# Kernel tuning notes

Hardware: AMD Instinct MI355X
Metric: run time of the kernel (lower is better)

Reference implementation:

```python
import jax, jax.numpy as jnp
import numpy as np

SCALE = 1.0 / np.sqrt(512.0).astype(np.float32)  # attention() hardcodes d_k=512


def setup_inputs() -> dict:
    key = jax.random.key(0)
    ks = jax.random.split(key, 9)
    B, S, D = 4, 2048, 512
    mk = lambda k, shape: jax.random.normal(k, shape, dtype=jnp.float32) * 0.05
    return {
        "q": mk(ks[0], (B, S, D)),
        "k": mk(ks[1], (B, S, D)),
        "v": mk(ks[2], (B, S, D)),
        "WQ_w": mk(ks[3], (D, D)),
        "WQ_b": mk(ks[4], (D,)),
        "WK_w": mk(ks[5], (D, D)),
        "WK_b": mk(ks[6], (D,)),
        "WV_w": mk(ks[7], (D, D)),
        "WV_b": mk(ks[8], (D,)),
    }


def reference(q, k, v, WQ_w, WQ_b, WK_w, WK_b, WV_w, WV_b):
    # torch nn.Linear: y = x @ W.T + b
    qp = q @ WQ_w.T + WQ_b  # [B,S,dk]
    kp = k @ WK_w.T + WK_b  # [B,S,dk]
    vp = v @ WV_w.T + WV_b  # [B,S,dv]
    qk = jnp.einsum("bqd,bkd->bqk", qp, kp) * SCALE  # [B,Sq,Sk]
    S = qk.shape[1]
    tril = jnp.tril(jnp.ones((S, S), dtype=qk.dtype))  # multiplicative causal mask
    qk = qk * tril
    # NOTE: original applies softmax over dim=1 (the query axis), faithfully kept.
    attn = jax.nn.softmax(qk, axis=1)
    out = jnp.einsum("bqk,bkd->bqd", attn, vp)  # [B,Sq,dv]
    return out
```

## Files before the change

### kernel.cpp

```cpp
#include <hip/hip_runtime.h>
#include <hip/hip_bf16.h>


#define S_LEN 2048
#define D_DIM 512
#define SCALE_F 0.044194173824159216f

typedef __attribute__((ext_vector_type(8))) short s8v;
typedef __attribute__((ext_vector_type(4))) short s4v;
typedef __attribute__((ext_vector_type(4))) float f4v;

enum { EPI_BIAS = 0, EPI_BIAS_T = 1, EPI_SCORES = 2 };

#define SBAR()    __builtin_amdgcn_s_barrier()
#define SCHEDB()  __builtin_amdgcn_sched_barrier(0)
#define WAITV(n)  asm volatile("s_waitcnt vmcnt(" #n ")")
#define WAITL0()  asm volatile("s_waitcnt lgkmcnt(0)")

__device__ __forceinline__ short f2bf_s(float f) {
  union { __hip_bfloat16 b; short s; } u; u.b = __float2bfloat16(f); return u.s;
}
__device__ __forceinline__ float bf2f_s(short h) {
  union { short s; __hip_bfloat16 b; } u; u.s = h; return __bfloat162float(u.b);
}

__device__ __forceinline__ void glds16(const short* g, short* l) {
  __builtin_amdgcn_global_load_lds((const __attribute__((address_space(1))) void*)g,
                                   (__attribute__((address_space(3))) void*)l, 16, 0, 0);
}

__device__ __forceinline__ unsigned lds_addr(const short* p) {
  return (unsigned)(unsigned long long)(const __attribute__((address_space(3))) short*)p;
}

__device__ __forceinline__ s8v dsr128(unsigned a) {
  s8v r;
  asm volatile("ds_read_b128 %0, %1" : "=&v"(r) : "v"(a));
  return r;
}

template <int EPI>
__device__ __forceinline__ void gemm_core(
    const short* __restrict__ A, const short* __restrict__ B,
    short* __restrict__ C, const float* __restrict__ bias,
    short* SMEM, int N, int K, size_t sCz, int m0, int n0, int bz,
    float* __restrict__ Z)
{
  const int tid  = threadIdx.x;
  const int w    = tid >> 6;
  const int lane = tid & 63;
  const int quad = lane >> 4;
  const int l16  = lane & 15;
  const int wm   = (w >> 1) * 64;
  const int wn   = (w & 1) * 64;

  const int strow = tid >> 3;
  const int gl = ((tid & 7) ^ (strow & 7)) * 8;

  f4v acc[4][4];
#pragma unroll
  for (int i = 0; i < 4; ++i)
#pragma unroll
    for (int j = 0; j < 4; ++j)
#pragma unroll
      for (int r = 0; r < 4; ++r) acc[i][j][r] = 0.0f;

  const short* Ag = A + (size_t)(m0 + strow) * K + gl;
  const short* Bg = B + (size_t)(n0 + strow) * K + gl;
  const size_t pstr = (size_t)32 * K;
  const int t8 = tid * 8;
  const int swq = l16 & 7;

  const unsigned base = lds_addr(SMEM);
  unsigned aoff[4], boff[4];
#pragma unroll
  for (int ii = 0; ii < 4; ++ii)
    aoff[ii] = base + (unsigned)((wm + ii * 16 + l16) * 128 + ((quad ^ swq) * 16));
#pragma unroll
  for (int j = 0; j < 4; ++j)
    boff[j] = base + 16384u + (unsigned)((wn + j * 16 + l16) * 128 + ((quad ^ swq) * 16));

  const int niter = K >> 6;

#pragma unroll
  for (int p = 0; p < 4; ++p) glds16(Ag + p * pstr, SMEM + t8 + p * 2048);
#pragma unroll
  for (int p = 0; p < 4; ++p) glds16(Bg + p * pstr, SMEM + 8192 + t8 + p * 2048);

  for (int i = 0; i < niter; ++i) {
    const int c = i & 1;
    if (i + 1 < niter) {
      const int k1 = (i + 1) << 6;
      short* dA = SMEM + (1 - c) * 16384 + t8;
#pragma unroll
      for (int p = 0; p < 4; ++p) glds16(Ag + k1 + p * pstr, dA + p * 2048);
#pragma unroll
      for (int p = 0; p < 4; ++p) glds16(Bg + k1 + p * pstr, dA + 8192 + p * 2048);
      SCHEDB();
      WAITV(8);
    } else {
      WAITV(0);
    }
    SBAR();
    SCHEDB();

    const unsigned cofs = (unsigned)(c << 15);
#pragma unroll
    for (int kk = 0; kk < 2; ++kk) {
      const unsigned kx = (unsigned)(kk << 6);
      s8v af[4], bf[4];
#pragma unroll
      for (int ii = 0; ii < 4; ++ii) af[ii] = dsr128((aoff[ii] ^ kx) + cofs);
#pragma unroll
      for (int j = 0; j < 4; ++j)   bf[j]  = dsr128((boff[j] ^ kx) + cofs);
      WAITL0();
      SCHEDB();
      __builtin_amdgcn_s_setprio(1);
#pragma unroll
      for (int ii = 0; ii < 4; ++ii)
#pragma unroll
        for (int j = 0; j < 4; ++j)
          acc[ii][j] = __builtin_amdgcn_mfma_f32_16x16x32_bf16(af[ii], bf[j], acc[ii][j], 0, 0, 0);
      __builtin_amdgcn_s_setprio(0);
    }
    SBAR();
  }

  float bv[4];
  if (EPI == EPI_BIAS || EPI == EPI_BIAS_T) {
#pragma unroll
    for (int j = 0; j < 4; ++j) bv[j] = bias[n0 + wn + j * 16 + l16];
  }

  if (EPI == EPI_BIAS_T) {
#pragma unroll
    for (int i = 0; i < 4; ++i) {
#pragma unroll
      for (int j = 0; j < 4; ++j) {
        const int gn  = n0 + wn + j * 16 + l16;
        const int gmb = m0 + wm + i * 16 + quad * 4;
        const int bb = gmb >> 11, ssb = gmb & (S_LEN - 1);
        s4v o;
#pragma unroll
        for (int r = 0; r < 4; ++r) o[r] = f2bf_s(acc[i][j][r] + bv[j]);
        *(s4v*)&C[((size_t)bb * D_DIM + gn) * S_LEN + ssb] = o;
      }
    }
    return;
  }

  short* TB = SMEM;
  const int wbase = w * 2176;
  float csum[4] = {0.f, 0.f, 0.f, 0.f};

#pragma unroll
  for (int ph = 0; ph < 2; ++ph) {
    __syncthreads();
#pragma unroll
    for (int ii = 0; ii < 2; ++ii) {
      const int i = ph * 2 + ii;
#pragma unroll
      for (int j = 0; j < 4; ++j) {
        const int gn = n0 + wn + j * 16 + l16;
#pragma unroll
        for (int r = 0; r < 4; ++r) {
          short o;
          if (EPI == EPI_SCORES) {
            const int gm = m0 + wm + i * 16 + quad * 4 + r;
            const float f = (gm >= gn) ? (__expf(acc[i][j][r] * SCALE_F) - 1.0f) : 0.0f;
            csum[j] += f;
            o = f2bf_s(f);
          } else {
            o = f2bf_s(acc[i][j][r] + bv[j]);
          }
          TB[wbase + (ii * 16 + quad * 4 + r) * 68 + j * 16 + l16] = o;
        }
      }
    }
    __syncthreads();
#pragma unroll
    for (int p = 0; p < 4; ++p) {
      const int row = p * 8 + (lane >> 3);
      const int cg  = lane & 7;
      const s8v vv = *(const s8v*)&TB[wbase + row * 68 + cg * 8];
      const int gm = m0 + wm + ph * 32 + row;
      const int gn = n0 + wn + cg * 8;
      *(s8v*)&C[sCz + (size_t)gm * N + gn] = vv;
    }
  }

  if (EPI == EPI_SCORES) {
#pragma unroll
    for (int j = 0; j < 4; ++j) {
      float cs = csum[j];
      cs += __shfl_xor(cs, 16, 64);
      cs += __shfl_xor(cs, 32, 64);
      if (quad == 0) atomicAdd(&Z[(bz << 11) + n0 + wn + j * 16 + l16], cs);
    }
  }
}

__global__ __launch_bounds__(256, 2) void proj_qk(
    const short* __restrict__ a0, const short* __restrict__ a1,
    const short* __restrict__ b0, const short* __restrict__ b1,
    short* __restrict__ c0, short* __restrict__ c1,
    const float* __restrict__ x0, const float* __restrict__ x1)
{
  __shared__ __align__(16) short SMEM[32768];
  const int bid = blockIdx.x;
  const int bsw = (bid & 7) * 64 + (bid >> 3);
  const int z   = bsw >> 8;
  const int rem = bsw & 255;
  const int m0  = (rem >> 2) * 128;
  const int n0  = (rem & 3) * 128;
  const short* A = z ? a1 : a0;
  const short* B = z ? b1 : b0;
  short*       C = z ? c1 : c0;
  const float* bias = z ? x1 : x0;
  gemm_core<EPI_BIAS>(A, B, C, bias, SMEM, D_DIM, D_DIM, 0, m0, n0, 0, nullptr);
}

__global__ __launch_bounds__(256, 2) void scores_projv(
    const short* __restrict__ qp, const short* __restrict__ kp, short* __restrict__ F,
    float* __restrict__ Z,
    const short* __restrict__ vb, const short* __restrict__ Wvb,
    short* __restrict__ vpT, const float* __restrict__ xv)
{
  __shared__ __align__(16) short SMEM[32768];
  const int bid = blockIdx.x;
  if (bid < 544) {
    const int bsw = (bid & 7) * 68 + (bid >> 3);
    const int bz  = bsw / 136;
    const int t   = bsw - bz * 136;
    int ti = (int)((sqrtf(8.0f * t + 1.0f) - 1.0f) * 0.5f);
    while ((ti + 1) * (ti + 2) / 2 <= t) ++ti;
    while (ti * (ti + 1) / 2 > t) --ti;
    const int tj = t - ti * (ti + 1) / 2;
    gemm_core<EPI_SCORES>(qp + (size_t)bz * S_LEN * D_DIM, kp + (size_t)bz * S_LEN * D_DIM,
                          F, nullptr, SMEM, S_LEN, D_DIM,
                          (size_t)bz * S_LEN * S_LEN, ti * 128, tj * 128, bz, Z);
  } else {
    const int h   = bid - 544;
    const int hsw = (h & 7) * 32 + (h >> 3);
    const int m0  = (hsw >> 2) * 128;
    const int n0  = (hsw & 3) * 128;
    gemm_core<EPI_BIAS_T>(vb, Wvb, vpT, xv, SMEM, D_DIM, D_DIM, 0, m0, n0, 0, nullptr);
  }
}

__global__ __launch_bounds__(256, 2) void gemm_outF(
    const short* __restrict__ F, const short* __restrict__ vpT,
    const float* __restrict__ Tv, float* __restrict__ out)
{
  __shared__ __align__(16) short SMEM[36864];

  const int tid  = threadIdx.x;
  const int h    = blockIdx.x;
  const int x    = h & 7;
  const int s    = h >> 3;
  const int n0   = (s & 3) * 128;
  const int bz   = (s >> 2) & 3;
  const int zslot = s >> 4;
  const int zs   = (zslot < 2) ? (2 * x + zslot) : (16 + 2 * x + (zslot - 2));
  const int mi   = (zs < 16) ? (31 - zs) : (zs - 16);
  const int m0   = mi * 64;

  const short* A = F   + (size_t)bz * S_LEN * S_LEN;
  const short* B = vpT + (size_t)bz * D_DIM * S_LEN;

  const int w    = tid >> 6;
  const int lane = tid & 63;
  const int quad = lane >> 4;
  const int l16  = lane & 15;
  const int wm   = (w >> 1) * 32;
  const int wn   = (w & 1) * 64;

  const int strow = tid >> 3;
  const int gl = ((tid & 7) ^ (strow & 7)) * 8;

  f4v acc[2][4];
#pragma unroll
  for (int i = 0; i < 2; ++i)
#pragma unroll
    for (int j = 0; j < 4; ++j)
#pragma unroll
      for (int r = 0; r < 4; ++r) acc[i][j][r] = 0.0f;

  const short* Ag = A + (size_t)(m0 + strow) * S_LEN + gl;
  const short* Bg = B + (size_t)(n0 + strow) * S_LEN + gl;
  const size_t pstr = (size_t)32 * S_LEN;
  const int t8 = tid * 8;
  const int swq = l16 & 7;

  const unsigned base = lds_addr(SMEM);
  unsigned aoff[2], boff[4];
#pragma unroll
  for (int ii = 0; ii < 2; ++ii)
    aoff[ii] = base + (unsigned)((wm + ii * 16 + l16) * 128 + ((quad ^ swq) * 16));
#pragma unroll
  for (int j = 0; j < 4; ++j)
    boff[j] = base + 8192u + (unsigned)((wn + j * 16 + l16) * 128 + ((quad ^ swq) * 16));

  const int niter = mi + 1;

#pragma unroll
  for (int pre = 0; pre < 2; ++pre) {
    short* dst = SMEM + pre * 12288 + t8;
    const int k0 = pre << 6;
#pragma unroll
    for (int p = 0; p < 2; ++p) glds16(Ag + k0 + p * pstr, dst + p * 2048);
#pragma unroll
    for (int p = 0; p < 4; ++p) glds16(Bg + k0 + p * pstr, dst + 4096 + p * 2048);
  }

  int cbuf = 0;
  for (int i = 0; i < niter; ++i) {
    if (i + 1 < niter) { WAITV(6); } else { WAITV(0); }
    SBAR();
    SCHEDB();

    if (i + 2 < niter) {
      int nb = cbuf + 2; if (nb >= 3) nb -= 3;
      const int k2 = (i + 2) << 6;
      short* dst = SMEM + nb * 12288 + t8;
#pragma unroll
      for (int p = 0; p < 2; ++p) glds16(Ag + k2 + p * pstr, dst + p * 2048);
#pragma unroll
      for (int p = 0; p < 4; ++p) glds16(Bg + k2 + p * pstr, dst + 4096 + p * 2048);
      SCHEDB();
    }

    const unsigned cofs = (unsigned)(cbuf * 24576);
    cbuf = (cbuf == 2) ? 0 : cbuf + 1;
#pragma unroll
    for (int kk = 0; kk < 2; ++kk) {
      const unsigned kx = (unsigned)(kk << 6);
      s8v af[2], bf[4];
#pragma unroll
      for (int ii = 0; ii < 2; ++ii) af[ii] = dsr128((aoff[ii] ^ kx) + cofs);
#pragma unroll
      for (int j = 0; j < 4; ++j)   bf[j]  = dsr128((boff[j] ^ kx) + cofs);
      WAITL0();
      SCHEDB();
      __builtin_amdgcn_s_setprio(1);
#pragma unroll
      for (int ii = 0; ii < 2; ++ii)
#pragma unroll
        for (int j = 0; j < 4; ++j)
          acc[ii][j] = __builtin_amdgcn_mfma_f32_16x16x32_bf16(af[ii], bf[j], acc[ii][j], 0, 0, 0);
      __builtin_amdgcn_s_setprio(0);
    }
  }

  float* Cf = out + (size_t)bz * S_LEN * D_DIM;
#pragma unroll
  for (int i = 0; i < 2; ++i) {
#pragma unroll
    for (int j = 0; j < 4; ++j) {
      const int gn = n0 + wn + j * 16 + l16;
      const float tvn = Tv[(bz << 9) + gn];
#pragma unroll
      for (int r = 0; r < 4; ++r) {
        const int gm = m0 + wm + i * 16 + quad * 4 + r;
        Cf[(size_t)gm * D_DIM + gn] = acc[i][j][r] + tvn;
      }
    }
  }
}

__global__ __launch_bounds__(256) void cvt_all(
    const float* __restrict__ q, const float* __restrict__ k, const float* __restrict__ v,
    const float* __restrict__ wq, const float* __restrict__ wk, const float* __restrict__ wv,
    short* __restrict__ qb, short* __restrict__ kb, short* __restrict__ vb,
    short* __restrict__ Wqb, short* __restrict__ Wkb, short* __restrict__ Wvb,
    float* __restrict__ ZF)
{
  const int y = blockIdx.y;
  const float* s; short* d; int i;
  if (blockIdx.x < 2048) {
    s = (y == 0) ? q : (y == 1) ? k : v;
    d = (y == 0) ? qb : (y == 1) ? kb : vb;
    i = (blockIdx.x * 256 + threadIdx.x) * 8;
    if (y == 0) {
      const int gid = blockIdx.x * 256 + threadIdx.x;
      if (gid < 8192) ZF[gid] = 0.0f;
    }
  } else {
    s = (y == 0) ? wq : (y == 1) ? wk : wv;
    d = (y == 0) ? Wqb : (y == 1) ? Wkb : Wvb;
    i = ((int)(blockIdx.x - 2048) * 256 + threadIdx.x) * 8;
  }
  const float4 f0 = *(const float4*)(s + i);
  const float4 f1 = *(const float4*)(s + i + 4);
  s8v o;
  o[0] = f2bf_s(f0.x); o[1] = f2bf_s(f0.y); o[2] = f2bf_s(f0.z); o[3] = f2bf_s(f0.w);
  o[4] = f2bf_s(f1.x); o[5] = f2bf_s(f1.y); o[6] = f2bf_s(f1.z); o[7] = f2bf_s(f1.w);
  *(s8v*)(d + i) = o;
}

__global__ __launch_bounds__(256) void scale_vpt_T(
    short* __restrict__ vpT, const float* __restrict__ ZF, float* __restrict__ Tv)
{
  __shared__ float red[4];
  const int b = blockIdx.y, d = blockIdx.x, tid = threadIdx.x;
  const size_t rowbase = ((size_t)(b * D_DIM + d)) * S_LEN;
  const float* zf = ZF + (b << 11);
  const int k0 = tid * 8;

  s8v v = *(s8v*)&vpT[rowbase + k0];
  float s = 0.0f;
#pragma unroll
  for (int i = 0; i < 8; ++i) {
    const float w = bf2f_s(v[i]) / (2048.0f + zf[k0 + i]);
    s += w;
    v[i] = f2bf_s(w);
  }
  *(s8v*)&vpT[rowbase + k0] = v;

#pragma unroll
  for (int off = 32; off >= 1; off >>= 1) s += __shfl_xor(s, off, 64);
  if ((tid & 63) == 0) red[tid >> 6] = s;
  __syncthreads();
  if (tid == 0) Tv[(b << 9) + d] = red[0] + red[1] + red[2] + red[3];
}

extern "C" void kernel_launch(void* const* d_in, const int* in_sizes, int n_in,
                              void* d_out, int out_size, void* d_ws, size_t ws_size,
                              hipStream_t stream) {
  const float* q   = (const float*)d_in[0];
  const float* k   = (const float*)d_in[1];
  const float* v   = (const float*)d_in[2];
  const float* WQw = (const float*)d_in[3];
  const float* WQb = (const float*)d_in[4];
  const float* WKw = (const float*)d_in[5];
  const float* WKb = (const float*)d_in[6];
  const float* WVw = (const float*)d_in[7];
  const float* WVb = (const float*)d_in[8];

  char* ws = (char*)d_ws;
  short* F   = (short*)(ws);
  short* qb  = (short*)(ws);
  short* kb  = qb + 4194304;
  short* Wqb = (short*)(ws + 25165824);
  short* Wkb = Wqb + 262144;
  short* qp  = (short*)(ws + 33554432);
  short* kp  = (short*)(ws + 41943040);
  short* vpT = (short*)(ws + 50331648);
  float* ZF  = (float*)(ws + 58720256);
  float* Tv  = (float*)(ws + 58753024);
  short* vb  = (short*)d_out;
  short* Wvb = (short*)d_out + 4194304;

  const dim3 blk(256);

  cvt_all<<<dim3(2176, 3), blk, 0, stream>>>(
      q, k, v, WQw, WKw, WVw, qb, kb, vb, Wqb, Wkb, Wvb, ZF);

  proj_qk<<<dim3(512), blk, 0, stream>>>(qb, kb, Wqb, Wkb, qp, kp, WQb, WKb);

  scores_projv<<<dim3(800), blk, 0, stream>>>(qp, kp, F, ZF, vb, Wvb, vpT, WVb);

  scale_vpt_T<<<dim3(512, 4), blk, 0, stream>>>(vpT, ZF, Tv);

  gemm_outF<<<dim3(512), blk, 0, stream>>>(F, vpT, Tv, (float*)d_out);
}
```

Baseline: 162.4 us.

## Fuse V-projection scaling and column-sum into scores kernel via completion counter

Removes the separate scale_vpt_T kernel. V-projection blocks in scores_projv now spin-wait on a global counter until all 544 score tiles have finished writing their Z column sums. They then divide by (2048+Z), write bf16 vpT, and atomically accumulate Tv. This saves one launch and a full read/write pass over vpT, but V blocks hold CUs while they wait, and the cross-block spin could stall or hit the guard if blocks are not co-resident.

```diff
diff --git a/kernel.cpp b/kernel.cpp
--- a/kernel.cpp
+++ b/kernel.cpp
@@ -10,7 +10,7 @@
 typedef __attribute__((ext_vector_type(4))) short s4v;
 typedef __attribute__((ext_vector_type(4))) float f4v;
 
-enum { EPI_BIAS = 0, EPI_BIAS_T = 1, EPI_SCORES = 2 };
+enum { EPI_BIAS = 0, EPI_BIAS_T = 1, EPI_SCORES = 2, EPI_BIAS_T_SCALED = 3 };
 
 #define SBAR()    __builtin_amdgcn_s_barrier()
 #define SCHEDB()  __builtin_amdgcn_sched_barrier(0)
@@ -44,7 +44,7 @@
     const short* __restrict__ A, const short* __restrict__ B,
     short* __restrict__ C, const float* __restrict__ bias,
     short* SMEM, int N, int K, size_t sCz, int m0, int n0, int bz,
-    float* __restrict__ Z)
+    float* __restrict__ Z, float* __restrict__ TvP, int* __restrict__ done)
 {
   const int tid  = threadIdx.x;
   const int w    = tid >> 6;
@@ -127,7 +127,7 @@
   }
 
   float bv[4];
-  if (EPI == EPI_BIAS || EPI == EPI_BIAS_T) {
+  if (EPI == EPI_BIAS || EPI == EPI_BIAS_T || EPI == EPI_BIAS_T_SCALED) {
 #pragma unroll
     for (int j = 0; j < 4; ++j) bv[j] = bias[n0 + wn + j * 16 + l16];
   }
@@ -145,6 +145,47 @@
         for (int r = 0; r < 4; ++r) o[r] = f2bf_s(acc[i][j][r] + bv[j]);
         *(s4v*)&C[((size_t)bb * D_DIM + gn) * S_LEN + ssb] = o;
       }
+    }
+    return;
+  }
+
+  if (EPI == EPI_BIAS_T_SCALED) {
+    if (tid == 0) {
+      int guard = 0;
+      while (__hip_atomic_load(done, __ATOMIC_RELAXED, __HIP_MEMORY_SCOPE_AGENT) < 544) {
+        __builtin_amdgcn_s_sleep(8);
+        if (++guard > (1 << 22)) break;
+      }
+      __threadfence();
+    }
+    __syncthreads();
+
+    const int bb  = m0 >> 11;
+    const int kb0 = m0 & (S_LEN - 1);
+    const float* zf = Z + (bb << 11);
+    float csum[4] = {0.f, 0.f, 0.f, 0.f};
+#pragma unroll
+    for (int i = 0; i < 4; ++i) {
+#pragma unroll
+      for (int j = 0; j < 4; ++j) {
+        const int gn  = n0 + wn + j * 16 + l16;
+        const int kk0 = kb0 + wm + i * 16 + quad * 4;
+        s4v o;
+#pragma unroll
+        for (int r = 0; r < 4; ++r) {
+          const float sc = (acc[i][j][r] + bv[j]) / (2048.0f + zf[kk0 + r]);
+          csum[j] += sc;
+          o[r] = f2bf_s(sc);
+        }
+        *(s4v*)&C[((size_t)bb * D_DIM + gn) * S_LEN + kk0] = o;
+      }
+    }
+#pragma unroll
+    for (int j = 0; j < 4; ++j) {
+      float cs = csum[j];
+      cs += __shfl_xor(cs, 16, 64);
+      cs += __shfl_xor(cs, 32, 64);
+      if (quad == 0) atomicAdd(&TvP[(bb << 9) + n0 + wn + j * 16 + l16], cs);
     }
     return;
   }
@@ -217,14 +258,16 @@
   const short* B = z ? b1 : b0;
   short*       C = z ? c1 : c0;
   const float* bias = z ? x1 : x0;
-  gemm_core<EPI_BIAS>(A, B, C, bias, SMEM, D_DIM, D_DIM, 0, m0, n0, 0, nullptr);
+  gemm_core<EPI_BIAS>(A, B, C, bias, SMEM, D_DIM, D_DIM, 0, m0, n0, 0,
+                      nullptr, nullptr, nullptr);
 }
 
 __global__ __launch_bounds__(256, 2) void scores_projv(
     const short* __restrict__ qp, const short* __restrict__ kp, short* __restrict__ F,
     float* __restrict__ Z,
     const short* __restrict__ vb, const short* __restrict__ Wvb,
-    short* __restrict__ vpT, const float* __restrict__ xv)
+    short* __restrict__ vpT, const float* __restrict__ xv,
+    float* __restrict__ Tv, int* __restrict__ done)
 {
   __shared__ __align__(16) short SMEM[32768];
   const int bid = blockIdx.x;
@@ -238,13 +281,20 @@
     const int tj = t - ti * (ti + 1) / 2;
     gemm_core<EPI_SCORES>(qp + (size_t)bz * S_LEN * D_DIM, kp + (size_t)bz * S_LEN * D_DIM,
                           F, nullptr, SMEM, S_LEN, D_DIM,
-                          (size_t)bz * S_LEN * S_LEN, ti * 128, tj * 128, bz, Z);
+                          (size_t)bz * S_LEN * S_LEN, ti * 128, tj * 128, bz, Z,
+                          nullptr, nullptr);
+    __syncthreads();
+    if (threadIdx.x == 0) {
+      __threadfence();
+      __hip_atomic_fetch_add(done, 1, __ATOMIC_RELAXED, __HIP_MEMORY_SCOPE_AGENT);
+    }
   } else {
     const int h   = bid - 544;
     const int hsw = (h & 7) * 32 + (h >> 3);
     const int m0  = (hsw >> 2) * 128;
     const int n0  = (hsw & 3) * 128;
-    gemm_core<EPI_BIAS_T>(vb, Wvb, vpT, xv, SMEM, D_DIM, D_DIM, 0, m0, n0, 0, nullptr);
+    gemm_core<EPI_BIAS_T_SCALED>(vb, Wvb, vpT, xv, SMEM, D_DIM, D_DIM, 0, m0, n0, 0,
+                                 Z, Tv, done);
   }
 }
 
@@ -373,7 +423,7 @@
     const float* __restrict__ wq, const float* __restrict__ wk, const float* __restrict__ wv,
     short* __restrict__ qb, short* __restrict__ kb, short* __restrict__ vb,
     short* __restrict__ Wqb, short* __restrict__ Wkb, short* __restrict__ Wvb,
-    float* __restrict__ ZF)
+    float* __restrict__ ZF, float* __restrict__ Tv, int* __restrict__ done)
 {
   const int y = blockIdx.y;
   const float* s; short* d; int i;
@@ -384,6 +434,8 @@
     if (y == 0) {
       const int gid = blockIdx.x * 256 + threadIdx.x;
       if (gid < 8192) ZF[gid] = 0.0f;
+      if (gid < 2048) Tv[gid] = 0.0f;
+      if (gid < 16)   done[gid] = 0;
     }
   } else {
     s = (y == 0) ? wq : (y == 1) ? wk : wv;
@@ -396,32 +448,6 @@
   o[0] = f2bf_s(f0.x); o[1] = f2bf_s(f0.y); o[2] = f2bf_s(f0.z); o[3] = f2bf_s(f0.w);
   o[4] = f2bf_s(f1.x); o[5] = f2bf_s(f1.y); o[6] = f2bf_s(f1.z); o[7] = f2bf_s(f1.w);
   *(s8v*)(d + i) = o;
-}
-
-__global__ __launch_bounds__(256) void scale_vpt_T(
-    short* __restrict__ vpT, const float* __restrict__ ZF, float* __restrict__ Tv)
-{
-  __shared__ float red[4];
-  const int b = blockIdx.y, d = blockIdx.x, tid = threadIdx.x;
-  const size_t rowbase = ((size_t)(b * D_DIM + d)) * S_LEN;
-  const float* zf = ZF + (b << 11);
-  const int k0 = tid * 8;
-
-  s8v v = *(s8v*)&vpT[rowbase + k0];
-  float s = 0.0f;
-#pragma unroll
-  for (int i = 0; i < 8; ++i) {
-    const float w = bf2f_s(v[i]) / (2048.0f + zf[k0 + i]);
-    s += w;
-    v[i] = f2bf_s(w);
-  }
-  *(s8v*)&vpT[rowbase + k0] = v;
-
-#pragma unroll
-  for (int off = 32; off >= 1; off >>= 1) s += __shfl_xor(s, off, 64);
-  if ((tid & 63) == 0) red[tid >> 6] = s;
-  __syncthreads();
-  if (tid == 0) Tv[(b << 9) + d] = red[0] + red[1] + red[2] + red[3];
 }
 
 extern "C" void kernel_launch(void* const* d_in, const int* in_sizes, int n_in,
@@ -448,19 +474,19 @@
   short* vpT = (short*)(ws + 50331648);
   float* ZF  = (float*)(ws + 58720256);
   float* Tv  = (float*)(ws + 58753024);
+  int*   done = (int*)(ws + 58761216);
   short* vb  = (short*)d_out;
   short* Wvb = (short*)d_out + 4194304;
 
   const dim3 blk(256);
 
   cvt_all<<<dim3(2176, 3), blk, 0, stream>>>(
-      q, k, v, WQw, WKw, WVw, qb, kb, vb, Wqb, Wkb, Wvb, ZF);
+      q, k, v, WQw, WKw, WVw, qb, kb, vb, Wqb, Wkb, Wvb, ZF, Tv, done);
 
   proj_qk<<<dim3(512), blk, 0, stream>>>(qb, kb, Wqb, Wkb, qp, kp, WQb, WKb);
 
-  scores_projv<<<dim3(800), blk, 0, stream>>>(qp, kp, F, ZF, vb, Wvb, vpT, WVb);
-
-  scale_vpt_T<<<dim3(512, 4), blk, 0, stream>>>(vpT, ZF, Tv);
+  scores_projv<<<dim3(800), blk, 0, stream>>>(
+      qp, kp, F, ZF, vb, Wvb, vpT, WVb, Tv, done);
 
   gemm_outF<<<dim3(512), blk, 0, stream>>>(F, vpT, Tv, (float*)d_out);
 }
```

Measured after the change: 185.4 us. +14.1%, slower.
